# Performance work log

Hardware: AMD Instinct MI355X
Metric: run time of the kernel (lower is better)

The kernel has to match this reference:

```python
import jax, jax.numpy as jnp
import numpy as np

FEAT_DIM = 128
GUIDE_DIM = 128
NIR_DIM = 32
H_LR, W_LR = 128, 128
H_HR, W_HR = 256, 256
IMNET_IN = FEAT_DIM + 2 * GUIDE_DIM + 2  # 386


def make_coord_1d(n):
    # pixel-center coords in [-1, 1]: (2i+1)/n - 1
    return (2.0 * jnp.arange(n, dtype=jnp.float32) + 1.0) / n - 1.0


def nearest_sample(img, cy, cx):
    """F.grid_sample(img, grid, mode='nearest', align_corners=False, padding='zeros').
    img: [b, C, h, w]; cy, cx: [N] normalized coords (cy -> h axis, cx -> w axis).
    Returns sampled values [b, C, N] and the pixel-center coords (qcy, qcx) the
    nearest sample corresponds to (0 when out of range, matching zero padding)."""
    h, w = img.shape[-2], img.shape[-1]
    iy = jnp.round(((cy + 1.0) * h - 1.0) * 0.5).astype(jnp.int32)  # round-half-even == nearbyint
    ix = jnp.round(((cx + 1.0) * w - 1.0) * 0.5).astype(jnp.int32)
    valid = (iy >= 0) & (iy < h) & (ix >= 0) & (ix < w)
    iyc = jnp.clip(iy, 0, h - 1)
    ixc = jnp.clip(ix, 0, w - 1)
    out = img[:, :, iyc, ixc]                       # [b, C, N] gather
    out = jnp.where(valid[None, None, :], out, 0.0)
    qcy = jnp.where(valid, (2.0 * iyc.astype(jnp.float32) + 1.0) / h - 1.0, 0.0)
    qcx = jnp.where(valid, (2.0 * ixc.astype(jnp.float32) + 1.0) / w - 1.0, 0.0)
    return out, qcy, qcx


def mlp(x, W1, b1, W2, b2, W3, b3):
    x = jax.nn.relu(x @ W1 + b1)
    x = jax.nn.relu(x @ W2 + b2)
    return x @ W3 + b3


def setup_inputs() -> dict:
    key = jax.random.key(0)
    ks = jax.random.split(key, 9)
    return {
        "feat": jax.random.normal(ks[0], (1, FEAT_DIM, H_LR, W_LR), jnp.float32),
        "lr_guide": jax.random.normal(ks[1], (1, GUIDE_DIM, H_LR, W_LR), jnp.float32),
        "hr_guide": jax.random.normal(ks[2], (1, GUIDE_DIM, H_HR, W_HR), jnp.float32),
        "W1": jax.random.normal(ks[3], (IMNET_IN, 256), jnp.float32) * 0.05,
        "b1": jax.random.normal(ks[4], (256,), jnp.float32) * 0.05,
        "W2": jax.random.normal(ks[5], (256, 128), jnp.float32) * 0.05,
        "b2": jax.random.normal(ks[6], (128,), jnp.float32) * 0.05,
        "W3": jax.random.normal(ks[7], (128, NIR_DIM), jnp.float32) * 0.05,
        "b3": jax.random.normal(ks[8], (NIR_DIM,), jnp.float32) * 0.05,
    }


def reference(feat, lr_guide, hr_guide, W1, b1, W2, b2, W3, b3):
    b, _, h, w = feat.shape
    _, cg, H, W = hr_guide.shape
    N = H * W
    featc = jnp.concatenate([lr_guide, feat], axis=1)        # [b, guide+feat, h, w]

    gy, gx = jnp.meshgrid(make_coord_1d(H), make_coord_1d(W), indexing="ij")
    cy = gy.reshape(-1)                                      # [N] coord[:, 0] (h axis)
    cx = gx.reshape(-1)                                      # [N] coord[:, 1] (w axis)

    q_guide_hr = hr_guide.reshape(b, cg, N).transpose(0, 2, 1)  # [b, N, cg]

    # feat_ : gather at the unshifted coord (identical across neighbors)
    feat_b, _, _ = nearest_sample(featc, cy, cx)
    feat_b = feat_b.transpose(0, 2, 1)                       # [b, N, C]

    rx = 1.0 / h
    ry = 1.0 / w
    preds, gcs = [], []
    for vx in (-1.0, 1.0):
        for vy in (-1.0, 1.0):
            q_feat, qcy, qcx = nearest_sample(featc, cy + vx * rx, cx + vy * ry)
            q_feat = q_feat.transpose(0, 2, 1)               # [b, N, C]
            rel = jnp.stack([(cy - qcy) * h, (cx - qcx) * w], axis=-1)  # [N, 2]
            rel = jnp.broadcast_to(rel[None], (b, N, 2))
            inp = jnp.concatenate([q_feat, q_guide_hr, rel], axis=-1)  # [b, N, 386]
            preds.append(mlp(inp, W1, b1, W2, b2, W3, b3))   # [b, N, NIR]
            # bilateral color weight: dot over channels [-4:-1]
            gcs.append(jnp.sum(feat_b[..., -4:-1] * q_feat[..., -4:-1], axis=-1))
    preds = jnp.stack(preds, axis=-1)                        # [b, N, NIR, 4]
    weight = jax.nn.softmax(jnp.stack(gcs, axis=-1), axis=-1)  # [b, N, 4]
    ret = jnp.sum(preds * weight[:, :, None, :], axis=-1)    # [b, N, NIR]
    return ret.transpose(0, 2, 1).reshape(b, -1, H, W)
```

## Files before the change

### kernel.cpp

```cpp
#include <hip/hip_runtime.h>
#include <hip/hip_bf16.h>


using bf16x8 = __attribute__((ext_vector_type(8))) __bf16;
using f32x4  = __attribute__((ext_vector_type(4))) float;

__device__ __forceinline__ float bf2f(unsigned short u){
  unsigned int x = ((unsigned int)u) << 16;
  return __builtin_bit_cast(float, x);
}
__device__ __forceinline__ unsigned short f2bf(float f){
  unsigned int x = __builtin_bit_cast(unsigned int, f);
  unsigned int r = x + 0x7fffu + ((x >> 16) & 1u);
  return (unsigned short)(r >> 16);
}
__device__ __forceinline__ bf16x8 ld8(const ushort* p){
  uint4 r = *(const uint4*)p;
  return __builtin_bit_cast(bf16x8, r);
}

struct RowMeta { int valid, ix; float relY, relX; int spos; };
__device__ __forceinline__ RowMeta row_meta(int Y, int X, int br){
  int ivx = br >> 1, ivy = br & 1;
  int validY, iy; float relY;
  if (ivx == 0){ validY = (Y >= 1);   iy = (Y-1) >> 1; relY = (Y & 1) ?  0.5f :  1.5f; }
  else         { validY = (Y <= 254); iy = (Y+1) >> 1; relY = (Y & 1) ? -1.5f : -0.5f; }
  int validX, ix; float relX;
  if (ivy == 0){ validX = (X >= 1);   ix = (X-1) >> 1; relX = (X & 1) ?  0.5f :  1.5f; }
  else         { validX = (X <= 254); ix = (X+1) >> 1; relX = (X & 1) ? -1.5f : -0.5f; }
  RowMeta r;
  r.valid = validY && validX;
  r.ix = ix;
  if (r.valid){ r.relY = relY; r.relX = relX; r.spos = iy*128 + ix; }
  else { r.relY = (float)Y + 0.5f - 128.0f; r.relX = (float)X + 0.5f - 128.0f; r.spos = -1; }
  return r;
}

__global__ __launch_bounds__(256) void convert_weights(
    const float* __restrict__ W1, const float* __restrict__ b1,
    const float* __restrict__ W2, const float* __restrict__ W3,
    ushort* __restrict__ W1t,
    ushort* __restrict__ W2t,
    ushort* __restrict__ W3t,
    ushort* __restrict__ Wx,
    ushort* __restrict__ Ubz)
{
  int b = blockIdx.x, t = threadIdx.x;
  if (b < 256){
    W1t[b*384 + t] = f2bf(W1[t*256 + b]);
    if (t < 128) W1t[b*384 + 256 + t] = f2bf(W1[(256+t)*256 + b]);
    if (t < 32){
      float v = (t==0) ? W1[384*256 + b] : (t==1) ? W1[385*256 + b]
              : (t==2) ? b1[b] : 0.0f;
      Wx[b*32 + t] = f2bf(v);
    }
    if (b < 128) W2t[b*256 + t] = f2bf(W2[t*128 + b]);
    if (b < 32 && t < 128) W3t[b*128 + t] = f2bf(W3[t*32 + b]);
  } else {
    Ubz[t] = 0;
  }
}

__global__ __launch_bounds__(256) void stage1_gemm(
    const float* __restrict__ src0, const float* __restrict__ src1,
    const ushort* __restrict__ W1t,
    ushort* __restrict__ outp)
{
  __shared__ ushort A[32*136];
  const int t = threadIdx.x;
  const int w = t >> 6, lane = t & 63, quad = lane >> 4, l15 = lane & 15;
  const int pos0  = (blockIdx.x >> 1) * 32;
  const int nside = (blockIdx.x & 1) * 128;
  const int mt = w >> 1;
  const int ntb = (w & 1) * 4;

  f32x4 acc[4];
  #pragma unroll
  for (int nt=0; nt<4; nt++) acc[nt] = f32x4{0.f,0.f,0.f,0.f};

  for (int h=0; h<2; h++){
    const float* src = h ? src1 : src0;
    #pragma unroll
    for (int i=0; i<16; i++){
      int f = i*256 + t;
      int k = f >> 5, mm = f & 31;
      A[mm*136 + k] = f2bf(src[(size_t)k*16384 + pos0 + mm]);
    }
    __syncthreads();
    #pragma unroll
    for (int kt=0; kt<4; kt++){
      bf16x8 a = ld8(&A[(mt*16 + l15)*136 + kt*32 + quad*8]);
      #pragma unroll
      for (int nt=0; nt<4; nt++){
        bf16x8 b = ld8(&W1t[(size_t)(nside + (ntb+nt)*16 + l15)*384 + h*128 + kt*32 + quad*8]);
        acc[nt] = __builtin_amdgcn_mfma_f32_16x16x32_bf16(a, b, acc[nt], 0,0,0);
      }
    }
    __syncthreads();
  }
  #pragma unroll
  for (int nt=0; nt<4; nt++){
    int n = nside + (ntb+nt)*16 + l15;
    #pragma unroll
    for (int r=0; r<4; r++){
      int mm = mt*16 + quad*4 + r;
      outp[(size_t)(pos0 + mm)*256 + n] = f2bf(acc[nt][r]);
    }
  }
}

__global__ __launch_bounds__(256, 4) void main_fused(
    const float* __restrict__ feat,
    const float* __restrict__ hr_guide,
    const float* __restrict__ b2v,
    const float* __restrict__ b3v,
    const ushort* __restrict__ Ub,
    const ushort* __restrict__ W1t,
    const ushort* __restrict__ Wx,
    const ushort* __restrict__ W2t,
    const ushort* __restrict__ W3t,
    float* __restrict__ outp)
{
  __shared__ __align__(16) ushort A1[64*264];
  __shared__ __align__(16) ushort Ahr[16*136];
  __shared__ float gcs[64];
  __shared__ float wgt[64];

  const int t = threadIdx.x;
  const int w = t >> 6, lane = t & 63, quad = lane >> 4, l15 = lane & 15;
  const int Y  = blockIdx.x >> 4;
  const int X0 = (blockIdx.x & 15) << 4;

  if (t < 64){
    RowMeta g = row_meta(Y, X0 + (t>>2), t & 3);
    float gc = 0.0f;
    if (g.spos >= 0){
      int bpos = (Y>>1)*128 + ((X0 + (t>>2)) >> 1);
      #pragma unroll
      for (int cc=0; cc<3; cc++)
        gc += feat[(size_t)(124+cc)*16384 + bpos] * feat[(size_t)(124+cc)*16384 + g.spos];
    }
    gcs[t] = gc;
  }
  #pragma unroll
  for (int i=0; i<2; i++){
    int id = i*256 + t;
    int ch = id >> 2, xq = id & 3;
    float4 v = *(const float4*)(hr_guide + (size_t)ch*65536 + Y*256 + X0 + xq*4);
    Ahr[(xq*4+0)*136 + ch] = f2bf(v.x);
    Ahr[(xq*4+1)*136 + ch] = f2bf(v.y);
    Ahr[(xq*4+2)*136 + ch] = f2bf(v.z);
    Ahr[(xq*4+3)*136 + ch] = f2bf(v.w);
  }
  bf16x8 b2f[8][2];
  #pragma unroll
  for (int kt=0; kt<4; kt++)
    #pragma unroll
    for (int nt=0; nt<2; nt++)
      b2f[kt][nt] = ld8(&W2t[(size_t)(w*32 + nt*16 + l15)*256 + kt*32 + quad*8]);

  RowMeta rmct[4]; int urow[4];
  #pragma unroll
  for (int ct=0; ct<4; ct++){
    int m = 16*ct + l15;
    rmct[ct] = row_meta(Y, X0 + (m>>2), m & 3);
    urow[ct] = rmct[ct].spos >= 0 ? rmct[ct].spos : 16387;
  }
  bf16x8 bk3[4];
  #pragma unroll
  for (int ct=0; ct<4; ct++){
    union { bf16x8 v; ushort s[8]; } bb;
    #pragma unroll
    for (int j=0; j<8; j++){
      int s = quad*8 + j;
      unsigned short val = 0;
      if (s == 0) val = f2bf(rmct[ct].relY);
      else if (s == 1) val = f2bf(rmct[ct].relX);
      else if (s == 2) val = 0x3F80u;
      bb.s[j] = val;
    }
    bk3[ct] = bb.v;
  }
  __syncthreads();
  if (t < 16){
    float g0 = gcs[t*4+0], g1 = gcs[t*4+1], g2 = gcs[t*4+2], g3 = gcs[t*4+3];
    float mx = fmaxf(fmaxf(g0,g1), fmaxf(g2,g3));
    float e0 = __expf(g0-mx), e1 = __expf(g1-mx), e2 = __expf(g2-mx), e3 = __expf(g3-mx);
    float inv = 1.0f/(e0+e1+e2+e3);
    wgt[t*4+0]=e0*inv; wgt[t*4+1]=e1*inv; wgt[t*4+2]=e2*inv; wgt[t*4+3]=e3*inv;
  }

  #pragma unroll
  for (int i=0; i<4; i++){
    int n = w*64 + i*16 + l15;
    const ushort* wp = W1t + (size_t)n*384 + 256;
    bf16x8 a0 = ld8(wp + 0*32 + quad*8);
    bf16x8 a1 = ld8(wp + 1*32 + quad*8);
    bf16x8 a2 = ld8(wp + 2*32 + quad*8);
    bf16x8 a3 = ld8(wp + 3*32 + quad*8);
    bf16x8 a4 = ld8(&Wx[(size_t)n*32 + quad*8]);
    int ncol0 = w*64 + i*16 + quad*4;
    uint2 u4[4];
    #pragma unroll
    for (int ct=0; ct<4; ct++)
      u4[ct] = *(const uint2*)&Ub[(size_t)urow[ct]*256 + ncol0];
    #pragma unroll
    for (int ct=0; ct<4; ct++){
      const ushort* hp = &Ahr[(4*ct + (l15>>2))*136 + quad*8];
      f32x4 acc = f32x4{0.f,0.f,0.f,0.f};
      acc = __builtin_amdgcn_mfma_f32_16x16x32_bf16(a0, ld8(hp +  0), acc, 0,0,0);
      acc = __builtin_amdgcn_mfma_f32_16x16x32_bf16(a1, ld8(hp + 32), acc, 0,0,0);
      acc = __builtin_amdgcn_mfma_f32_16x16x32_bf16(a2, ld8(hp + 64), acc, 0,0,0);
      acc = __builtin_amdgcn_mfma_f32_16x16x32_bf16(a3, ld8(hp + 96), acc, 0,0,0);
      acc = __builtin_amdgcn_mfma_f32_16x16x32_bf16(a4, bk3[ct], acc, 0,0,0);
      union { uint2 v; ushort s[4]; } uu; uu.v = u4[ct];
      int mrow = 16*ct + l15;
      uint2 o;
      o.x = (unsigned)f2bf(fmaxf(acc[0] + bf2f(uu.s[0]), 0.f))
          | ((unsigned)f2bf(fmaxf(acc[1] + bf2f(uu.s[1]), 0.f)) << 16);
      o.y = (unsigned)f2bf(fmaxf(acc[2] + bf2f(uu.s[2]), 0.f))
          | ((unsigned)f2bf(fmaxf(acc[3] + bf2f(uu.s[3]), 0.f)) << 16);
      *(uint2*)&A1[mrow*264 + ncol0] = o;
    }
  }
  __syncthreads();

  #pragma unroll
  for (int kt=4; kt<8; kt++)
    #pragma unroll
    for (int nt=0; nt<2; nt++)
      b2f[kt][nt] = ld8(&W2t[(size_t)(w*32 + nt*16 + l15)*256 + kt*32 + quad*8]);

  f32x4 acc2[4][2];
  #pragma unroll
  for (int mt=0; mt<4; mt++)
    #pragma unroll
    for (int nt=0; nt<2; nt++) acc2[mt][nt] = f32x4{0.f,0.f,0.f,0.f};
  #pragma unroll
  for (int kt=0; kt<8; kt++)
    #pragma unroll
    for (int mt=0; mt<4; mt++){
      bf16x8 a = ld8(&A1[(mt*16 + l15)*264 + kt*32 + quad*8]);
      #pragma unroll
      for (int nt=0; nt<2; nt++)
        acc2[mt][nt] = __builtin_amdgcn_mfma_f32_16x16x32_bf16(a, b2f[kt][nt], acc2[mt][nt], 0,0,0);
    }

  bf16x8 b3f[4][2];
  #pragma unroll
  for (int kt=0; kt<4; kt++)
    #pragma unroll
    for (int nt=0; nt<2; nt++)
      b3f[kt][nt] = ld8(&W3t[(size_t)(nt*16 + l15)*128 + kt*32 + quad*8]);
  __syncthreads();

  {
    ushort* A2 = A1;
    float bias0 = b2v[w*32 + l15], bias1 = b2v[w*32 + 16 + l15];
    #pragma unroll
    for (int mt=0; mt<4; mt++)
      #pragma unroll
      for (int nt=0; nt<2; nt++){
        int n = w*32 + nt*16 + l15;
        float bv = nt ? bias1 : bias0;
        #pragma unroll
        for (int r=0; r<4; r++){
          int mm = mt*16 + quad*4 + r;
          A2[mm*136 + n] = f2bf(fmaxf(acc2[mt][nt][r] + bv, 0.0f));
        }
      }
  }
  __syncthreads();

  {
    const ushort* A2 = A1;
    f32x4 acc3[2] = { f32x4{0.f,0.f,0.f,0.f}, f32x4{0.f,0.f,0.f,0.f} };
    #pragma unroll
    for (int kt=0; kt<4; kt++){
      bf16x8 a = ld8(&A2[(w*16 + l15)*136 + kt*32 + quad*8]);
      #pragma unroll
      for (int nt=0; nt<2; nt++)
        acc3[nt] = __builtin_amdgcn_mfma_f32_16x16x32_bf16(a, b3f[kt][nt], acc3[nt], 0,0,0);
    }
    int lp = w*4 + quad;
    int X = X0 + lp;
    float w0 = wgt[lp*4+0], w1 = wgt[lp*4+1], w2 = wgt[lp*4+2], w3 = wgt[lp*4+3];
    #pragma unroll
    for (int nt=0; nt<2; nt++){
      int n = nt*16 + l15;
      float bb = b3v[n];
      float v = w0*(acc3[nt][0]+bb) + w1*(acc3[nt][1]+bb)
              + w2*(acc3[nt][2]+bb) + w3*(acc3[nt][3]+bb);
      outp[(size_t)n*65536 + (size_t)Y*256 + X] = v;
    }
  }
}

extern "C" void kernel_launch(void* const* d_in, const int* in_sizes, int n_in,
                              void* d_out, int out_size, void* d_ws, size_t ws_size,
                              hipStream_t stream)
{
  const float* feat     = (const float*)d_in[0];
  const float* lr_guide = (const float*)d_in[1];
  const float* hr_guide = (const float*)d_in[2];
  const float* W1       = (const float*)d_in[3];
  const float* b1       = (const float*)d_in[4];
  const float* W2       = (const float*)d_in[5];
  const float* b2       = (const float*)d_in[6];
  const float* W3       = (const float*)d_in[7];
  const float* b3       = (const float*)d_in[8];
  float* outp = (float*)d_out;

  char* ws = (char*)d_ws;
  ushort* W1t = (ushort*)(ws);
  ushort* W2t = (ushort*)(ws + 196608);
  ushort* W3t = (ushort*)(ws + 262144);
  ushort* Wx  = (ushort*)(ws + 270336);
  ushort* Ub  = (ushort*)(ws + 286720);
  ushort* Ubz = Ub + (size_t)16387*256;

  convert_weights<<<257, 256, 0, stream>>>(W1, b1, W2, W3, W1t, W2t, W3t, Wx, Ubz);
  stage1_gemm<<<1024, 256, 0, stream>>>(lr_guide, feat, W1t, Ub);
  main_fused<<<4096, 256, 0, stream>>>(feat, hr_guide, b2, b3,
                                       Ub, W1t, Wx, W2t, W3t, outp);
}
```

Measured before the change: 233.1 us.

## Process four rows per block with register-resident weights and software-prefetched tiles

main_fused now handles four consecutive output rows per block, so the grid shrinks from 4096 to 1024 blocks. W1/Wx/W2 fragments are loaded into registers once per block and reused across the rows. The next row's Ub rows, hr_guide tile and bilateral features are prefetched into registers while the current row's second GEMM runs, with double-buffered softmax weights. Separately, the weight conversion kernel is reorganized for coalesced reads and stage1 loads use float4. The extra live registers may reduce occupancy under launch_bounds(256,4), and fewer blocks means less parallelism.

```diff
diff --git a/kernel.cpp b/kernel.cpp
--- a/kernel.cpp
+++ b/kernel.cpp
@@ -46,16 +46,20 @@
     ushort* __restrict__ Ubz)
 {
   int b = blockIdx.x, t = threadIdx.x;
-  if (b < 256){
-    W1t[b*384 + t] = f2bf(W1[t*256 + b]);
-    if (t < 128) W1t[b*384 + 256 + t] = f2bf(W1[(256+t)*256 + b]);
-    if (t < 32){
-      float v = (t==0) ? W1[384*256 + b] : (t==1) ? W1[385*256 + b]
-              : (t==2) ? b1[b] : 0.0f;
-      Wx[b*32 + t] = f2bf(v);
-    }
-    if (b < 128) W2t[b*256 + t] = f2bf(W2[t*128 + b]);
-    if (b < 32 && t < 128) W3t[b*128 + t] = f2bf(W3[t*32 + b]);
+  if (b < 384){
+    W1t[t*384 + b] = f2bf(W1[b*256 + t]);
+  } else if (b < 386){
+    Wx[t*32 + (b - 384)] = f2bf(W1[b*256 + t]);
+  } else if (b == 386){
+    Wx[t*32 + 2] = f2bf(b1[t]);
+    #pragma unroll
+    for (int j=3; j<32; j++) Wx[t*32 + j] = 0;
+  } else if (b < 387 + 256){
+    int k = b - 387;
+    if (t < 128) W2t[t*256 + k] = f2bf(W2[k*128 + t]);
+  } else if (b < 643 + 128){
+    int k = b - 643;
+    if (t < 32) W3t[t*128 + k] = f2bf(W3[k*32 + t]);
   } else {
     Ubz[t] = 0;
   }
@@ -81,10 +85,14 @@
   for (int h=0; h<2; h++){
     const float* src = h ? src1 : src0;
     #pragma unroll
-    for (int i=0; i<16; i++){
-      int f = i*256 + t;
-      int k = f >> 5, mm = f & 31;
-      A[mm*136 + k] = f2bf(src[(size_t)k*16384 + pos0 + mm]);
+    for (int j=0; j<4; j++){
+      int k  = (t >> 3) + j*32;
+      int mm = (t & 7) * 4;
+      float4 v = *(const float4*)(src + (size_t)k*16384 + pos0 + mm);
+      A[(mm+0)*136 + k] = f2bf(v.x);
+      A[(mm+1)*136 + k] = f2bf(v.y);
+      A[(mm+2)*136 + k] = f2bf(v.z);
+      A[(mm+3)*136 + k] = f2bf(v.w);
     }
     __syncthreads();
     #pragma unroll
@@ -124,175 +132,210 @@
   __shared__ __align__(16) ushort A1[64*264];
   __shared__ __align__(16) ushort Ahr[16*136];
   __shared__ float gcs[64];
-  __shared__ float wgt[64];
+  __shared__ float wgt[2][64];
 
   const int t = threadIdx.x;
   const int w = t >> 6, lane = t & 63, quad = lane >> 4, l15 = lane & 15;
-  const int Y  = blockIdx.x >> 4;
+  const int Y0 = (blockIdx.x >> 4) * 4;
   const int X0 = (blockIdx.x & 15) << 4;
 
-  if (t < 64){
-    RowMeta g = row_meta(Y, X0 + (t>>2), t & 3);
-    float gc = 0.0f;
-    if (g.spos >= 0){
-      int bpos = (Y>>1)*128 + ((X0 + (t>>2)) >> 1);
-      #pragma unroll
-      for (int cc=0; cc<3; cc++)
-        gc += feat[(size_t)(124+cc)*16384 + bpos] * feat[(size_t)(124+cc)*16384 + g.spos];
-    }
-    gcs[t] = gc;
-  }
-  #pragma unroll
-  for (int i=0; i<2; i++){
-    int id = i*256 + t;
-    int ch = id >> 2, xq = id & 3;
-    float4 v = *(const float4*)(hr_guide + (size_t)ch*65536 + Y*256 + X0 + xq*4);
-    Ahr[(xq*4+0)*136 + ch] = f2bf(v.x);
-    Ahr[(xq*4+1)*136 + ch] = f2bf(v.y);
-    Ahr[(xq*4+2)*136 + ch] = f2bf(v.z);
-    Ahr[(xq*4+3)*136 + ch] = f2bf(v.w);
-  }
+  bf16x8 a1f[4][4];
+  bf16x8 a4f[4];
   bf16x8 b2f[8][2];
   #pragma unroll
-  for (int kt=0; kt<4; kt++)
+  for (int i=0; i<4; i++){
+    int n = w*64 + i*16 + l15;
+    #pragma unroll
+    for (int kt=0; kt<4; kt++)
+      a1f[i][kt] = ld8(&W1t[(size_t)n*384 + 256 + kt*32 + quad*8]);
+    a4f[i] = ld8(&Wx[(size_t)n*32 + quad*8]);
+  }
+  #pragma unroll
+  for (int kt=0; kt<8; kt++)
     #pragma unroll
     for (int nt=0; nt<2; nt++)
       b2f[kt][nt] = ld8(&W2t[(size_t)(w*32 + nt*16 + l15)*256 + kt*32 + quad*8]);
 
-  RowMeta rmct[4]; int urow[4];
-  #pragma unroll
-  for (int ct=0; ct<4; ct++){
-    int m = 16*ct + l15;
-    rmct[ct] = row_meta(Y, X0 + (m>>2), m & 3);
-    urow[ct] = rmct[ct].spos >= 0 ? rmct[ct].spos : 16387;
-  }
-  bf16x8 bk3[4];
-  #pragma unroll
-  for (int ct=0; ct<4; ct++){
-    union { bf16x8 v; ushort s[8]; } bb;
-    #pragma unroll
-    for (int j=0; j<8; j++){
-      int s = quad*8 + j;
-      unsigned short val = 0;
-      if (s == 0) val = f2bf(rmct[ct].relY);
-      else if (s == 1) val = f2bf(rmct[ct].relX);
-      else if (s == 2) val = 0x3F80u;
-      bb.s[j] = val;
-    }
-    bk3[ct] = bb.v;
-  }
+  RowMeta rmct[4];
+  uint2   u4v[4][4];
+  float4  hrv[2];
+  float   gfa[3], gfb[3];
+  int     gvalid = 0;
+
+  auto prefetch_tile = [&](int Ycur){
+    int urow[4];
+    #pragma unroll
+    for (int ct=0; ct<4; ct++){
+      int m = 16*ct + l15;
+      rmct[ct] = row_meta(Ycur, X0 + (m>>2), m & 3);
+      urow[ct] = rmct[ct].spos >= 0 ? rmct[ct].spos : 16387;
+    }
+    #pragma unroll
+    for (int i=0; i<4; i++){
+      int nc = w*64 + i*16 + quad*4;
+      #pragma unroll
+      for (int ct=0; ct<4; ct++)
+        u4v[i][ct] = *(const uint2*)&Ub[(size_t)urow[ct]*256 + nc];
+    }
+    #pragma unroll
+    for (int i2=0; i2<2; i2++){
+      int id = i2*256 + t;
+      hrv[i2] = *(const float4*)(hr_guide + (size_t)(id>>2)*65536 + Ycur*256 + X0 + (id&3)*4);
+    }
+    if (t < 64){
+      RowMeta g = row_meta(Ycur, X0 + (t>>2), t & 3);
+      gvalid = g.spos >= 0;
+      int sp = gvalid ? g.spos : 0;
+      int bpos = (Ycur>>1)*128 + ((X0 + (t>>2)) >> 1);
+      #pragma unroll
+      for (int cc=0; cc<3; cc++){
+        gfa[cc] = feat[(size_t)(124+cc)*16384 + bpos];
+        gfb[cc] = feat[(size_t)(124+cc)*16384 + sp];
+      }
+    }
+  };
+  auto stage_tile = [&](){
+    #pragma unroll
+    for (int i2=0; i2<2; i2++){
+      int id = i2*256 + t;
+      int ch = id >> 2, xq = id & 3;
+      float4 v = hrv[i2];
+      Ahr[(xq*4+0)*136 + ch] = f2bf(v.x);
+      Ahr[(xq*4+1)*136 + ch] = f2bf(v.y);
+      Ahr[(xq*4+2)*136 + ch] = f2bf(v.z);
+      Ahr[(xq*4+3)*136 + ch] = f2bf(v.w);
+    }
+    if (t < 64)
+      gcs[t] = gvalid ? (gfa[0]*gfb[0] + gfa[1]*gfb[1] + gfa[2]*gfb[2]) : 0.0f;
+  };
+
+  prefetch_tile(Y0);
+  stage_tile();
   __syncthreads();
   if (t < 16){
     float g0 = gcs[t*4+0], g1 = gcs[t*4+1], g2 = gcs[t*4+2], g3 = gcs[t*4+3];
     float mx = fmaxf(fmaxf(g0,g1), fmaxf(g2,g3));
     float e0 = __expf(g0-mx), e1 = __expf(g1-mx), e2 = __expf(g2-mx), e3 = __expf(g3-mx);
     float inv = 1.0f/(e0+e1+e2+e3);
-    wgt[t*4+0]=e0*inv; wgt[t*4+1]=e1*inv; wgt[t*4+2]=e2*inv; wgt[t*4+3]=e3*inv;
-  }
-
-  #pragma unroll
-  for (int i=0; i<4; i++){
-    int n = w*64 + i*16 + l15;
-    const ushort* wp = W1t + (size_t)n*384 + 256;
-    bf16x8 a0 = ld8(wp + 0*32 + quad*8);
-    bf16x8 a1 = ld8(wp + 1*32 + quad*8);
-    bf16x8 a2 = ld8(wp + 2*32 + quad*8);
-    bf16x8 a3 = ld8(wp + 3*32 + quad*8);
-    bf16x8 a4 = ld8(&Wx[(size_t)n*32 + quad*8]);
-    int ncol0 = w*64 + i*16 + quad*4;
-    uint2 u4[4];
-    #pragma unroll
-    for (int ct=0; ct<4; ct++)
-      u4[ct] = *(const uint2*)&Ub[(size_t)urow[ct]*256 + ncol0];
+    wgt[0][t*4+0]=e0*inv; wgt[0][t*4+1]=e1*inv; wgt[0][t*4+2]=e2*inv; wgt[0][t*4+3]=e3*inv;
+  }
+
+  for (int s=0; s<4; s++){
+    const int Ycur = Y0 + s;
+
+    bf16x8 bk3[4];
     #pragma unroll
     for (int ct=0; ct<4; ct++){
-      const ushort* hp = &Ahr[(4*ct + (l15>>2))*136 + quad*8];
-      f32x4 acc = f32x4{0.f,0.f,0.f,0.f};
-      acc = __builtin_amdgcn_mfma_f32_16x16x32_bf16(a0, ld8(hp +  0), acc, 0,0,0);
-      acc = __builtin_amdgcn_mfma_f32_16x16x32_bf16(a1, ld8(hp + 32), acc, 0,0,0);
-      acc = __builtin_amdgcn_mfma_f32_16x16x32_bf16(a2, ld8(hp + 64), acc, 0,0,0);
-      acc = __builtin_amdgcn_mfma_f32_16x16x32_bf16(a3, ld8(hp + 96), acc, 0,0,0);
-      acc = __builtin_amdgcn_mfma_f32_16x16x32_bf16(a4, bk3[ct], acc, 0,0,0);
-      union { uint2 v; ushort s[4]; } uu; uu.v = u4[ct];
-      int mrow = 16*ct + l15;
-      uint2 o;
-      o.x = (unsigned)f2bf(fmaxf(acc[0] + bf2f(uu.s[0]), 0.f))
-          | ((unsigned)f2bf(fmaxf(acc[1] + bf2f(uu.s[1]), 0.f)) << 16);
-      o.y = (unsigned)f2bf(fmaxf(acc[2] + bf2f(uu.s[2]), 0.f))
-          | ((unsigned)f2bf(fmaxf(acc[3] + bf2f(uu.s[3]), 0.f)) << 16);
-      *(uint2*)&A1[mrow*264 + ncol0] = o;
-    }
-  }
-  __syncthreads();
-
-  #pragma unroll
-  for (int kt=4; kt<8; kt++)
-    #pragma unroll
-    for (int nt=0; nt<2; nt++)
-      b2f[kt][nt] = ld8(&W2t[(size_t)(w*32 + nt*16 + l15)*256 + kt*32 + quad*8]);
-
-  f32x4 acc2[4][2];
-  #pragma unroll
-  for (int mt=0; mt<4; mt++)
-    #pragma unroll
-    for (int nt=0; nt<2; nt++) acc2[mt][nt] = f32x4{0.f,0.f,0.f,0.f};
-  #pragma unroll
-  for (int kt=0; kt<8; kt++)
-    #pragma unroll
-    for (int mt=0; mt<4; mt++){
-      bf16x8 a = ld8(&A1[(mt*16 + l15)*264 + kt*32 + quad*8]);
+      union { bf16x8 v; ushort sh[8]; } bb;
+      #pragma unroll
+      for (int j=0; j<8; j++) bb.sh[j] = 0;
+      if (quad == 0){
+        bb.sh[0] = f2bf(rmct[ct].relY);
+        bb.sh[1] = f2bf(rmct[ct].relX);
+        bb.sh[2] = 0x3F80u;
+      }
+      bk3[ct] = bb.v;
+    }
+    #pragma unroll
+    for (int i=0; i<4; i++){
+      int ncol0 = w*64 + i*16 + quad*4;
+      #pragma unroll
+      for (int ct=0; ct<4; ct++){
+        const ushort* hp = &Ahr[(4*ct + (l15>>2))*136 + quad*8];
+        f32x4 acc = f32x4{0.f,0.f,0.f,0.f};
+        acc = __builtin_amdgcn_mfma_f32_16x16x32_bf16(a1f[i][0], ld8(hp +  0), acc, 0,0,0);
+        acc = __builtin_amdgcn_mfma_f32_16x16x32_bf16(a1f[i][1], ld8(hp + 32), acc, 0,0,0);
+        acc = __builtin_amdgcn_mfma_f32_16x16x32_bf16(a1f[i][2], ld8(hp + 64), acc, 0,0,0);
+        acc = __builtin_amdgcn_mfma_f32_16x16x32_bf16(a1f[i][3], ld8(hp + 96), acc, 0,0,0);
+        acc = __builtin_amdgcn_mfma_f32_16x16x32_bf16(a4f[i],    bk3[ct],      acc, 0,0,0);
+        union { uint2 v; ushort sh[4]; } uu; uu.v = u4v[i][ct];
+        int mrow = 16*ct + l15;
+        uint2 o;
+        o.x = (unsigned)f2bf(fmaxf(acc[0] + bf2f(uu.sh[0]), 0.f))
+            | ((unsigned)f2bf(fmaxf(acc[1] + bf2f(uu.sh[1]), 0.f)) << 16);
+        o.y = (unsigned)f2bf(fmaxf(acc[2] + bf2f(uu.sh[2]), 0.f))
+            | ((unsigned)f2bf(fmaxf(acc[3] + bf2f(uu.sh[3]), 0.f)) << 16);
+        *(uint2*)&A1[mrow*264 + ncol0] = o;
+      }
+    }
+    __syncthreads();
+
+    if (s < 3) prefetch_tile(Ycur + 1);
+
+    f32x4 acc2[4][2];
+    #pragma unroll
+    for (int mt=0; mt<4; mt++)
+      #pragma unroll
+      for (int nt=0; nt<2; nt++) acc2[mt][nt] = f32x4{0.f,0.f,0.f,0.f};
+    #pragma unroll
+    for (int mt=0; mt<4; mt++)
+      #pragma unroll
+      for (int kt=0; kt<8; kt++){
+        bf16x8 a = ld8(&A1[(mt*16 + l15)*264 + kt*32 + quad*8]);
+        #pragma unroll
+        for (int nt=0; nt<2; nt++)
+          acc2[mt][nt] = __builtin_amdgcn_mfma_f32_16x16x32_bf16(a, b2f[kt][nt], acc2[mt][nt], 0,0,0);
+      }
+    __syncthreads();
+
+    bf16x8 b3f[4][2];
+    #pragma unroll
+    for (int kt=0; kt<4; kt++)
       #pragma unroll
       for (int nt=0; nt<2; nt++)
-        acc2[mt][nt] = __builtin_amdgcn_mfma_f32_16x16x32_bf16(a, b2f[kt][nt], acc2[mt][nt], 0,0,0);
-    }
-
-  bf16x8 b3f[4][2];
-  #pragma unroll
-  for (int kt=0; kt<4; kt++)
-    #pragma unroll
-    for (int nt=0; nt<2; nt++)
-      b3f[kt][nt] = ld8(&W3t[(size_t)(nt*16 + l15)*128 + kt*32 + quad*8]);
-  __syncthreads();
-
-  {
-    ushort* A2 = A1;
-    float bias0 = b2v[w*32 + l15], bias1 = b2v[w*32 + 16 + l15];
-    #pragma unroll
-    for (int mt=0; mt<4; mt++)
+        b3f[kt][nt] = ld8(&W3t[(size_t)(nt*16 + l15)*128 + kt*32 + quad*8]);
+    {
+      ushort* A2 = A1;
+      float bias0 = b2v[w*32 + l15], bias1 = b2v[w*32 + 16 + l15];
+      #pragma unroll
+      for (int mt=0; mt<4; mt++)
+        #pragma unroll
+        for (int nt=0; nt<2; nt++){
+          int n = w*32 + nt*16 + l15;
+          float bv = nt ? bias1 : bias0;
+          #pragma unroll
+          for (int r=0; r<4; r++){
+            int mm = mt*16 + quad*4 + r;
+            A2[mm*136 + n] = f2bf(fmaxf(acc2[mt][nt][r] + bv, 0.0f));
+          }
+        }
+    }
+    if (s < 3) stage_tile();
+    __syncthreads();
+
+    {
+      const ushort* A2 = A1;
+      f32x4 acc3[2] = { f32x4{0.f,0.f,0.f,0.f}, f32x4{0.f,0.f,0.f,0.f} };
+      #pragma unroll
+      for (int kt=0; kt<4; kt++){
+        bf16x8 a = ld8(&A2[(w*16 + l15)*136 + kt*32 + quad*8]);
+        #pragma unroll
+        for (int nt=0; nt<2; nt++)
+          acc3[nt] = __builtin_amdgcn_mfma_f32_16x16x32_bf16(a, b3f[kt][nt], acc3[nt], 0,0,0);
+      }
+      int lp = w*4 + quad;
+      int X = X0 + lp;
+      const float* wp = wgt[s & 1];
+      float w0 = wp[lp*4+0], w1 = wp[lp*4+1], w2 = wp[lp*4+2], w3 = wp[lp*4+3];
       #pragma unroll
       for (int nt=0; nt<2; nt++){
-        int n = w*32 + nt*16 + l15;
-        float bv = nt ? bias1 : bias0;
-        #pragma unroll
-        for (int r=0; r<4; r++){
-          int mm = mt*16 + quad*4 + r;
-          A2[mm*136 + n] = f2bf(fmaxf(acc2[mt][nt][r] + bv, 0.0f));
-        }
-      }
-  }
-  __syncthreads();
-
-  {
-    const ushort* A2 = A1;
-    f32x4 acc3[2] = { f32x4{0.f,0.f,0.f,0.f}, f32x4{0.f,0.f,0.f,0.f} };
-    #pragma unroll
-    for (int kt=0; kt<4; kt++){
-      bf16x8 a = ld8(&A2[(w*16 + l15)*136 + kt*32 + quad*8]);
-      #pragma unroll
-      for (int nt=0; nt<2; nt++)
-        acc3[nt] = __builtin_amdgcn_mfma_f32_16x16x32_bf16(a, b3f[kt][nt], acc3[nt], 0,0,0);
-    }
-    int lp = w*4 + quad;
-    int X = X0 + lp;
-    float w0 = wgt[lp*4+0], w1 = wgt[lp*4+1], w2 = wgt[lp*4+2], w3 = wgt[lp*4+3];
-    #pragma unroll
-    for (int nt=0; nt<2; nt++){
-      int n = nt*16 + l15;
-      float bb = b3v[n];
-      float v = w0*(acc3[nt][0]+bb) + w1*(acc3[nt][1]+bb)
-              + w2*(acc3[nt][2]+bb) + w3*(acc3[nt][3]+bb);
-      outp[(size_t)n*65536 + (size_t)Y*256 + X] = v;
-    }
+        int n = nt*16 + l15;
+        float bb = b3v[n];
+        float v = w0*(acc3[nt][0]+bb) + w1*(acc3[nt][1]+bb)
+                + w2*(acc3[nt][2]+bb) + w3*(acc3[nt][3]+bb);
+        outp[(size_t)n*65536 + (size_t)Ycur*256 + X] = v;
+      }
+    }
+    if (s < 3 && t < 16){
+      float g0 = gcs[t*4+0], g1 = gcs[t*4+1], g2 = gcs[t*4+2], g3 = gcs[t*4+3];
+      float mx = fmaxf(fmaxf(g0,g1), fmaxf(g2,g3));
+      float e0 = __expf(g0-mx), e1 = __expf(g1-mx), e2 = __expf(g2-mx), e3 = __expf(g3-mx);
+      float inv = 1.0f/(e0+e1+e2+e3);
+      int nb = (s+1) & 1;
+      wgt[nb][t*4+0]=e0*inv; wgt[nb][t*4+1]=e1*inv;
+      wgt[nb][t*4+2]=e2*inv; wgt[nb][t*4+3]=e3*inv;
+    }
+    __syncthreads();
   }
 }
 
@@ -319,8 +362,8 @@
   ushort* Ub  = (ushort*)(ws + 286720);
   ushort* Ubz = Ub + (size_t)16387*256;
 
-  convert_weights<<<257, 256, 0, stream>>>(W1, b1, W2, W3, W1t, W2t, W3t, Wx, Ubz);
+  convert_weights<<<772, 256, 0, stream>>>(W1, b1, W2, W3, W1t, W2t, W3t, Wx, Ubz);
   stage1_gemm<<<1024, 256, 0, stream>>>(lr_guide, feat, W1t, Ub);
-  main_fused<<<4096, 256, 0, stream>>>(feat, hr_guide, b2, b3,
+  main_fused<<<1024, 256, 0, stream>>>(feat, hr_guide, b2, b3,
                                        Ub, W1t, Wx, W2t, W3t, outp);
 }
```

After: 430.0 us. 84.5% more time.
